# Performance work log

Measured on AMD Instinct MI355X. Metric: run time of the kernel, lower is better.

Reference implementation:

```python
import jax, jax.numpy as jnp
import numpy as np

EPS = 1e-6


def setup_inputs() -> dict:
    key = jax.random.key(0)
    k1, k2 = jax.random.split(key)
    inputs = jax.random.normal(k1, (32, 8, 256, 256), dtype=jnp.float32)
    targets = jax.random.uniform(k2, (32, 8, 256, 256), dtype=jnp.float32)
    return {"inputs": inputs, "targets": targets}


def reference(inputs, targets):
    # softmax over the class axis (dim=1), as in the torch module
    p = jax.nn.softmax(inputs, axis=1)
    B = p.shape[0]
    p = p.reshape(B, -1)          # [B, C*H*W]
    t = targets.reshape(B, -1)    # [B, C*H*W]
    # The torch loop iterates over every flattened column, summing over batch.
    inter = jnp.sum(p * t, axis=0)        # [C*H*W]
    denom = jnp.sum(p, axis=0) + jnp.sum(t, axis=0)  # [C*H*W]
    dice = jnp.sum((2.0 * inter + EPS) / (denom + EPS))
    num_cols = p.shape[1]
    return 1.0 - dice / num_cols
```

## Files before the change

### kernel.cpp

```cpp
#include <hip/hip_runtime.h>
#include <math.h>

constexpr int B_ = 32;
constexpr int C_ = 8;
constexpr int HW_ = 256 * 256;
constexpr float FEPS = 1e-6f;
constexpr float NUM_COLS = 8.0f * 65536.0f;

__global__ __launch_bounds__(256) void dice_main(const float* __restrict__ in,
                                                 const float* __restrict__ tg,
                                                 float* __restrict__ accum) {
    const int tid  = threadIdx.x;
    const int lane = tid & 63;
    const int bg   = tid >> 6;
    const int hw0  = blockIdx.x * 128 + lane * 2;

    float inter[2][8];
    float den[2][8];
#pragma unroll
    for (int v = 0; v < 2; ++v)
#pragma unroll
        for (int c = 0; c < 8; ++c) { inter[v][c] = 0.0f; den[v][c] = 0.0f; }

#pragma unroll
    for (int bi = 0; bi < 8; ++bi) {
        const int b = bg * 8 + bi;
        const int base = (b * C_) * HW_ + hw0;

        float2 xv[8], tv[8];
#pragma unroll
        for (int c = 0; c < 8; ++c) {
            xv[c] = *reinterpret_cast<const float2*>(in + base + c * HW_);
            tv[c] = *reinterpret_cast<const float2*>(tg + base + c * HW_);
        }

        float m0 = xv[0].x, m1 = xv[0].y;
#pragma unroll
        for (int c = 1; c < 8; ++c) { m0 = fmaxf(m0, xv[c].x); m1 = fmaxf(m1, xv[c].y); }

        float e0[8], e1[8];
        float s0 = 0.0f, s1 = 0.0f;
#pragma unroll
        for (int c = 0; c < 8; ++c) {
            e0[c] = __expf(xv[c].x - m0); s0 += e0[c];
            e1[c] = __expf(xv[c].y - m1); s1 += e1[c];
        }
        const float r0 = 1.0f / s0;
        const float r1 = 1.0f / s1;

#pragma unroll
        for (int c = 0; c < 8; ++c) {
            const float p0 = e0[c] * r0;
            const float p1 = e1[c] * r1;
            inter[0][c] = fmaf(p0, tv[c].x, inter[0][c]);
            inter[1][c] = fmaf(p1, tv[c].y, inter[1][c]);
            den[0][c] += p0 + tv[c].x;
            den[1][c] += p1 + tv[c].y;
        }
    }

    __shared__ float red[4][64][34];
#pragma unroll
    for (int v = 0; v < 2; ++v)
#pragma unroll
        for (int c = 0; c < 8; ++c) {
            red[bg][lane][v * 8 + c]      = inter[v][c];
            red[bg][lane][16 + v * 8 + c] = den[v][c];
        }
    __syncthreads();

    float part = 0.0f;
#pragma unroll
    for (int i = 0; i < 4; ++i) {
        const int j   = tid * 4 + i;
        const int lj  = j >> 4;
        const int idx = j & 15;
        const float it = red[0][lj][idx] + red[1][lj][idx] +
                         red[2][lj][idx] + red[3][lj][idx];
        const float dn = red[0][lj][16 + idx] + red[1][lj][16 + idx] +
                         red[2][lj][16 + idx] + red[3][lj][16 + idx];
        part += (2.0f * it + FEPS) / (dn + FEPS);
    }

#pragma unroll
    for (int off = 32; off > 0; off >>= 1)
        part += __shfl_down(part, off, 64);

    __shared__ float wsum[4];
    if (lane == 0) wsum[bg] = part;
    __syncthreads();
    if (tid == 0)
        atomicAdd(accum, wsum[0] + wsum[1] + wsum[2] + wsum[3]);
}

__global__ void dice_final(const float* __restrict__ accum, float* __restrict__ out) {
    out[0] = 1.0f - accum[0] * (1.0f / NUM_COLS);
}

extern "C" void kernel_launch(void* const* d_in, const int* in_sizes, int n_in,
                              void* d_out, int out_size, void* d_ws, size_t ws_size,
                              hipStream_t stream) {
    const float* in = (const float*)d_in[0];
    const float* tg = (const float*)d_in[1];
    float* out = (float*)d_out;
    float* acc = (float*)d_ws;

    hipMemsetAsync(acc, 0, sizeof(float), stream);
    dice_main<<<dim3(HW_ / 128), dim3(256), 0, stream>>>(in, tg, acc);
    dice_final<<<1, 1, 0, stream>>>(acc, out);
}
```

Baseline: 167.7 us.

## Use one pixel per thread, twice the blocks, LDS atomics, and a two-stage final reduction

Each thread now handles one pixel column instead of two, which doubles the grid to 1024 blocks and shrinks per-thread register state. The launch bound adds a minimum of 6 blocks per SM as an occupancy hint. The cross-batch-group LDS reduction becomes shared-memory atomics into a smaller array. The global float atomic and the memset are replaced by per-block partial sums that a 256-thread final kernel reduces. This is meant to raise occupancy and memory-level parallelism for a bandwidth-bound kernel. In exchange, loads are narrower scalar 4-byte accesses and LDS atomic contention is added.

Result: slower. 200.6 us (+19.6%).

```diff
diff --git a/kernel.cpp b/kernel.cpp
--- a/kernel.cpp
+++ b/kernel.cpp
@@ -1,100 +1,90 @@
 #include <hip/hip_runtime.h>
 #include <math.h>
 
-constexpr int B_ = 32;
-constexpr int C_ = 8;
 constexpr int HW_ = 256 * 256;
 constexpr float FEPS = 1e-6f;
 constexpr float NUM_COLS = 8.0f * 65536.0f;
 
-__global__ __launch_bounds__(256) void dice_main(const float* __restrict__ in,
-                                                 const float* __restrict__ tg,
-                                                 float* __restrict__ accum) {
+__global__ __launch_bounds__(256, 6) void dice_main(const float* __restrict__ in,
+                                                    const float* __restrict__ tg,
+                                                    float* __restrict__ partial) {
     const int tid  = threadIdx.x;
     const int lane = tid & 63;
     const int bg   = tid >> 6;
-    const int hw0  = blockIdx.x * 128 + lane * 2;
+    const int hw0  = blockIdx.x * 64 + lane;
 
-    float inter[2][8];
-    float den[2][8];
+    float inter[8], den[8];
 #pragma unroll
-    for (int v = 0; v < 2; ++v)
-#pragma unroll
-        for (int c = 0; c < 8; ++c) { inter[v][c] = 0.0f; den[v][c] = 0.0f; }
+    for (int c = 0; c < 8; ++c) { inter[c] = 0.0f; den[c] = 0.0f; }
 
 #pragma unroll
     for (int bi = 0; bi < 8; ++bi) {
-        const int b = bg * 8 + bi;
-        const int base = (b * C_) * HW_ + hw0;
+        const int b    = bg * 8 + bi;
+        const int base = b * 8 * HW_ + hw0;
 
-        float2 xv[8], tv[8];
+        float xv[8], tv[8];
 #pragma unroll
         for (int c = 0; c < 8; ++c) {
-            xv[c] = *reinterpret_cast<const float2*>(in + base + c * HW_);
-            tv[c] = *reinterpret_cast<const float2*>(tg + base + c * HW_);
+            xv[c] = in[base + c * HW_];
+            tv[c] = tg[base + c * HW_];
         }
 
-        float m0 = xv[0].x, m1 = xv[0].y;
+        float m = xv[0];
 #pragma unroll
-        for (int c = 1; c < 8; ++c) { m0 = fmaxf(m0, xv[c].x); m1 = fmaxf(m1, xv[c].y); }
+        for (int c = 1; c < 8; ++c) m = fmaxf(m, xv[c]);
 
-        float e0[8], e1[8];
-        float s0 = 0.0f, s1 = 0.0f;
+        float e[8], s = 0.0f;
 #pragma unroll
-        for (int c = 0; c < 8; ++c) {
-            e0[c] = __expf(xv[c].x - m0); s0 += e0[c];
-            e1[c] = __expf(xv[c].y - m1); s1 += e1[c];
-        }
-        const float r0 = 1.0f / s0;
-        const float r1 = 1.0f / s1;
+        for (int c = 0; c < 8; ++c) { e[c] = __expf(xv[c] - m); s += e[c]; }
+        const float r = 1.0f / s;
 
 #pragma unroll
         for (int c = 0; c < 8; ++c) {
-            const float p0 = e0[c] * r0;
-            const float p1 = e1[c] * r1;
-            inter[0][c] = fmaf(p0, tv[c].x, inter[0][c]);
-            inter[1][c] = fmaf(p1, tv[c].y, inter[1][c]);
-            den[0][c] += p0 + tv[c].x;
-            den[1][c] += p1 + tv[c].y;
+            const float p = e[c] * r;
+            inter[c] = fmaf(p, tv[c], inter[c]);
+            den[c]  += p + tv[c];
         }
     }
 
-    __shared__ float red[4][64][34];
+    __shared__ float red[64][17];
+    float* redf = &red[0][0];
+    for (int i = tid; i < 64 * 17; i += 256) redf[i] = 0.0f;
+    __syncthreads();
 #pragma unroll
-    for (int v = 0; v < 2; ++v)
-#pragma unroll
-        for (int c = 0; c < 8; ++c) {
-            red[bg][lane][v * 8 + c]      = inter[v][c];
-            red[bg][lane][16 + v * 8 + c] = den[v][c];
-        }
+    for (int c = 0; c < 8; ++c) {
+        atomicAdd(&red[lane][c],     inter[c]);
+        atomicAdd(&red[lane][8 + c], den[c]);
+    }
     __syncthreads();
 
     float part = 0.0f;
 #pragma unroll
-    for (int i = 0; i < 4; ++i) {
-        const int j   = tid * 4 + i;
-        const int lj  = j >> 4;
-        const int idx = j & 15;
-        const float it = red[0][lj][idx] + red[1][lj][idx] +
-                         red[2][lj][idx] + red[3][lj][idx];
-        const float dn = red[0][lj][16 + idx] + red[1][lj][16 + idx] +
-                         red[2][lj][16 + idx] + red[3][lj][16 + idx];
-        part += (2.0f * it + FEPS) / (dn + FEPS);
+    for (int k = 0; k < 2; ++k) {
+        const int j   = tid + k * 256;
+        const int hwi = j >> 3;
+        const int c   = j & 7;
+        part += (2.0f * red[hwi][c] + FEPS) / (red[hwi][8 + c] + FEPS);
     }
 
 #pragma unroll
-    for (int off = 32; off > 0; off >>= 1)
-        part += __shfl_down(part, off, 64);
+    for (int off = 32; off > 0; off >>= 1) part += __shfl_down(part, off, 64);
 
     __shared__ float wsum[4];
     if (lane == 0) wsum[bg] = part;
     __syncthreads();
-    if (tid == 0)
-        atomicAdd(accum, wsum[0] + wsum[1] + wsum[2] + wsum[3]);
+    if (tid == 0) partial[blockIdx.x] = wsum[0] + wsum[1] + wsum[2] + wsum[3];
 }
 
-__global__ void dice_final(const float* __restrict__ accum, float* __restrict__ out) {
-    out[0] = 1.0f - accum[0] * (1.0f / NUM_COLS);
+__global__ __launch_bounds__(256) void dice_final(const float* __restrict__ partial,
+                                                  float* __restrict__ out) {
+    const int tid = threadIdx.x;
+    float s = partial[tid] + partial[tid + 256] + partial[tid + 512] + partial[tid + 768];
+#pragma unroll
+    for (int off = 32; off > 0; off >>= 1) s += __shfl_down(s, off, 64);
+    __shared__ float ws[4];
+    if ((tid & 63) == 0) ws[tid >> 6] = s;
+    __syncthreads();
+    if (tid == 0) out[0] = 1.0f - (ws[0] + ws[1] + ws[2] + ws[3]) * (1.0f / NUM_COLS);
 }
 
 extern "C" void kernel_launch(void* const* d_in, const int* in_sizes, int n_in,
@@ -103,9 +93,8 @@
     const float* in = (const float*)d_in[0];
     const float* tg = (const float*)d_in[1];
     float* out = (float*)d_out;
-    float* acc = (float*)d_ws;
+    float* partial = (float*)d_ws;
 
-    hipMemsetAsync(acc, 0, sizeof(float), stream);
-    dice_main<<<dim3(HW_ / 128), dim3(256), 0, stream>>>(in, tg, acc);
-    dice_final<<<1, 1, 0, stream>>>(acc, out);
+    dice_main<<<dim3(1024), dim3(256), 0, stream>>>(in, tg, partial);
+    dice_final<<<dim3(1), dim3(256), 0, stream>>>(partial, out);
 }
```

## Use 512-thread blocks with 8 warps over batch and fuse finalization via counter

Applied to the files above, without the earlier changes.

Blocks now have 8 wavefronts, each covering 4 batch entries instead of 4 wavefronts covering 8, so each block has more memory loads in flight and a shorter serial loop per thread. The separate finalize kernel is dropped: the last block to finish, found with an atomic counter, computes the output, which saves one kernel launch. The shared reduction buffer is larger (8x64x33) and now uses 33-float row padding, which may limit occupancy, and the final step adds an atomic and a fence per block.

Result: no change. 165.1 us (-1.5%).

```diff
diff --git a/kernel.cpp b/kernel.cpp
--- a/kernel.cpp
+++ b/kernel.cpp
@@ -1,31 +1,30 @@
 #include <hip/hip_runtime.h>
 #include <math.h>
 
-constexpr int B_ = 32;
-constexpr int C_ = 8;
 constexpr int HW_ = 256 * 256;
 constexpr float FEPS = 1e-6f;
 constexpr float NUM_COLS = 8.0f * 65536.0f;
 
-__global__ __launch_bounds__(256) void dice_main(const float* __restrict__ in,
-                                                 const float* __restrict__ tg,
-                                                 float* __restrict__ accum) {
+__global__ __launch_bounds__(512, 4) void dice_main(const float* __restrict__ in,
+                                                    const float* __restrict__ tg,
+                                                    float* __restrict__ accum,
+                                                    unsigned int* __restrict__ counter,
+                                                    float* __restrict__ out) {
     const int tid  = threadIdx.x;
     const int lane = tid & 63;
-    const int bg   = tid >> 6;
+    const int w    = tid >> 6;
     const int hw0  = blockIdx.x * 128 + lane * 2;
 
-    float inter[2][8];
-    float den[2][8];
+    float inter[2][8], den[2][8];
 #pragma unroll
     for (int v = 0; v < 2; ++v)
 #pragma unroll
         for (int c = 0; c < 8; ++c) { inter[v][c] = 0.0f; den[v][c] = 0.0f; }
 
 #pragma unroll
-    for (int bi = 0; bi < 8; ++bi) {
-        const int b = bg * 8 + bi;
-        const int base = (b * C_) * HW_ + hw0;
+    for (int bi = 0; bi < 4; ++bi) {
+        const int b    = w * 4 + bi;
+        const int base = b * 8 * HW_ + hw0;
 
         float2 xv[8], tv[8];
 #pragma unroll
@@ -38,8 +37,7 @@
 #pragma unroll
         for (int c = 1; c < 8; ++c) { m0 = fmaxf(m0, xv[c].x); m1 = fmaxf(m1, xv[c].y); }
 
-        float e0[8], e1[8];
-        float s0 = 0.0f, s1 = 0.0f;
+        float e0[8], e1[8], s0 = 0.0f, s1 = 0.0f;
 #pragma unroll
         for (int c = 0; c < 8; ++c) {
             e0[c] = __expf(xv[c].x - m0); s0 += e0[c];
@@ -59,42 +57,52 @@
         }
     }
 
-    __shared__ float red[4][64][34];
+    __shared__ float red[8][64][33];
 #pragma unroll
     for (int v = 0; v < 2; ++v)
 #pragma unroll
         for (int c = 0; c < 8; ++c) {
-            red[bg][lane][v * 8 + c]      = inter[v][c];
-            red[bg][lane][16 + v * 8 + c] = den[v][c];
+            red[w][lane][v * 8 + c]      = inter[v][c];
+            red[w][lane][16 + v * 8 + c] = den[v][c];
         }
     __syncthreads();
 
     float part = 0.0f;
 #pragma unroll
-    for (int i = 0; i < 4; ++i) {
-        const int j   = tid * 4 + i;
-        const int lj  = j >> 4;
-        const int idx = j & 15;
-        const float it = red[0][lj][idx] + red[1][lj][idx] +
-                         red[2][lj][idx] + red[3][lj][idx];
-        const float dn = red[0][lj][16 + idx] + red[1][lj][16 + idx] +
-                         red[2][lj][16 + idx] + red[3][lj][16 + idx];
-        part += (2.0f * it + FEPS) / (dn + FEPS);
+    for (int i = 0; i < 2; ++i) {
+        const int j    = tid * 2 + i;
+        const int hw_l = j >> 3;
+        const int c    = j & 7;
+        const int ln   = hw_l >> 1;
+        const int v    = hw_l & 1;
+        float I = 0.0f, D = 0.0f;
+#pragma unroll
+        for (int ww = 0; ww < 8; ++ww) {
+            I += red[ww][ln][v * 8 + c];
+            D += red[ww][ln][16 + v * 8 + c];
+        }
+        part += (2.0f * I + FEPS) / (D + FEPS);
     }
 
 #pragma unroll
-    for (int off = 32; off > 0; off >>= 1)
-        part += __shfl_down(part, off, 64);
+    for (int off = 32; off > 0; off >>= 1) part += __shfl_down(part, off, 64);
 
-    __shared__ float wsum[4];
-    if (lane == 0) wsum[bg] = part;
+    __shared__ float wsum[8];
+    if (lane == 0) wsum[w] = part;
     __syncthreads();
-    if (tid == 0)
-        atomicAdd(accum, wsum[0] + wsum[1] + wsum[2] + wsum[3]);
-}
 
-__global__ void dice_final(const float* __restrict__ accum, float* __restrict__ out) {
-    out[0] = 1.0f - accum[0] * (1.0f / NUM_COLS);
+    if (tid == 0) {
+        float bs = 0.0f;
+#pragma unroll
+        for (int ww = 0; ww < 8; ++ww) bs += wsum[ww];
+        atomicAdd(accum, bs);
+        __threadfence();
+        const unsigned int done = atomicAdd(counter, 1u);
+        if (done == gridDim.x - 1) {
+            const float tot = atomicAdd(accum, 0.0f);
+            out[0] = 1.0f - tot * (1.0f / NUM_COLS);
+        }
+    }
 }
 
 extern "C" void kernel_launch(void* const* d_in, const int* in_sizes, int n_in,
@@ -103,9 +111,9 @@
     const float* in = (const float*)d_in[0];
     const float* tg = (const float*)d_in[1];
     float* out = (float*)d_out;
-    float* acc = (float*)d_ws;
+    float* accum = (float*)d_ws;
+    unsigned int* counter = (unsigned int*)d_ws + 1;
 
-    hipMemsetAsync(acc, 0, sizeof(float), stream);
-    dice_main<<<dim3(HW_ / 128), dim3(256), 0, stream>>>(in, tg, acc);
-    dice_final<<<1, 1, 0, stream>>>(acc, out);
+    hipMemsetAsync(d_ws, 0, 8, stream);
+    dice_main<<<dim3(HW_ / 128), dim3(512), 0, stream>>>(in, tg, accum, counter, out);
 }
```
